# Kernel tuning notes

Hardware: AMD Instinct MI355X
Metric: run time of the kernel (lower is better)

## Reference

```python
import jax, jax.numpy as jnp
from jax import lax
import numpy as np

SEARCH = 9          # search window (asserted == 9 in source)
PAD = SEARCH // 2   # 4
NUM_BINS = 10       # num_dist_bins
BIN_DISP = 0.5      # bin_displacement
NUM_ITER = 3        # num_iter
MIN_FILTER_REG = 1e-5


def _distance_map():
    # DistanceMap: soft-bin the radial distance from the window center.
    c = float(SEARCH // 2)
    yy, xx = jnp.meshgrid(jnp.arange(SEARCH, dtype=jnp.float32),
                          jnp.arange(SEARCH, dtype=jnp.float32), indexing='ij')
    d = jnp.sqrt((yy - c) ** 2 + (xx - c) ** 2) / BIN_DISP          # (9,9)
    k = jnp.arange(NUM_BINS, dtype=jnp.float32)
    bd = d[..., None] - k                                            # (9,9,B)
    vals = jnp.maximum(1.0 - jnp.abs(bd), 0.0)
    last = jnp.clip(bd[..., -1] + 1.0, 0.0, 1.0)                     # saturating last bin
    return vals.at[..., -1].set(last)                                # (9,9,B)


def _local_corr(f, ref_pad, disp):
    # f: (b,c,H,W); ref_pad: (b,c,H+8,W+8) -> scores (b,81,H,W)
    b, c, H, W = f.shape
    def step(_, d):
        r = lax.dynamic_slice(ref_pad, (0, 0, d[0], d[1]), (b, c, H, W))
        return None, jnp.einsum('bchw,bchw->bhw', f, r)
    _, out = lax.scan(step, None, disp)                              # (81,b,H,W)
    return jnp.moveaxis(out, 0, 1)


def _local_corr_t(res, ref_pad, disp):
    # res: (b,81,H,W) -> (b,c,H,W); adjoint of _local_corr w.r.t. the filter arg
    b, c = ref_pad.shape[0], ref_pad.shape[1]
    H, W = res.shape[2], res.shape[3]
    def step(acc, xs):
        d, rd = xs                                                   # rd: (b,H,W)
        r = lax.dynamic_slice(ref_pad, (0, 0, d[0], d[1]), (b, c, H, W))
        return acc + rd[:, None] * r, None
    acc0 = jnp.zeros((b, c, H, W), ref_pad.dtype)
    acc, _ = lax.scan(step, acc0, (disp, jnp.moveaxis(res, 1, 0)))
    return acc


def setup_inputs() -> dict:
    key = jax.random.key(0)
    k1, k2 = jax.random.split(key)
    b, c, H, W = 4, 128, 128, 128
    d = jnp.arange(NUM_BINS, dtype=jnp.float32) * BIN_DISP
    return {
        'filter_map': jax.random.normal(k1, (b, c, H, W), jnp.float32),
        'reference_feat': jax.random.normal(k2, (b, c, H, W), jnp.float32),
        # 1x1-conv predictor weights (num_bins -> 1), at their documented inits:
        'label_w': jnp.exp(-0.5 * d ** 2),            # init_gauss, sigma=1.0
        'spatial_w': jnp.ones((NUM_BINS,), jnp.float32),
        'mask_w': 4.0 * jnp.tanh(2.0 - d),            # v_minus_init_factor * tanh(2 - d)
        'log_step_length': jnp.zeros((1,), jnp.float32),   # log(1.0)
        'filter_reg': 0.01 * jnp.ones((1,), jnp.float32),
    }


def reference(filter_map, reference_feat, label_w, spatial_w, mask_w,
              log_step_length, filter_reg):
    b, c, H, W = filter_map.shape
    dm = _distance_map()                                             # (9,9,B)
    target_map = (dm @ label_w).reshape(1, SEARCH * SEARCH, 1, 1)
    v_plus = (dm @ spatial_w).reshape(1, SEARCH * SEARCH, 1, 1)
    weight_m = jax.nn.sigmoid(dm @ mask_w).reshape(1, SEARCH * SEARCH, 1, 1)

    step_length = jnp.exp(log_step_length).reshape(1, 1, 1, 1)
    reg_weight = jnp.maximum(filter_reg * filter_reg,
                             MIN_FILTER_REG ** 2).reshape(1, 1, 1, 1) / (c * c)

    dys, dxs = jnp.meshgrid(jnp.arange(SEARCH), jnp.arange(SEARCH), indexing='ij')
    disp = jnp.stack([dys.ravel(), dxs.ravel()], axis=1)             # (81,2)
    ref_pad = jnp.pad(reference_feat, ((0, 0), (0, 0), (PAD, PAD), (PAD, PAD)))

    # LeakyReluPar: f(s,a) = (1-a)/2*|s| + (1+a)/2*s ; deriv: (1-a)/2*sign(s) + (1+a)/2
    a_lo = (1.0 - weight_m) * 0.5
    a_hi = (1.0 + weight_m) * 0.5

    f = filter_map
    for _ in range(NUM_ITER):
        scores = _local_corr(f, ref_pad, disp)                       # (b,81,H,W)
        act = v_plus * (a_lo * jnp.abs(scores) + a_hi * scores)
        grad_act = v_plus * (a_lo * jnp.sign(scores) + a_hi)
        residuals = act - v_plus * target_map
        mapped = grad_act * residuals
        f_grad = reg_weight * f + _local_corr_t(mapped, ref_pad, disp)
        sg = grad_act * _local_corr(f_grad, ref_pad, disp)
        alpha_den = jnp.sum(sg * sg, axis=1, keepdims=True)          # (b,1,H,W)
        alpha_num = jnp.sum(f_grad * f_grad, axis=1, keepdims=True)
        alpha = alpha_num / jnp.maximum(alpha_den + reg_weight * alpha_num, 1e-8)
        f = f - step_length * alpha * f_grad
    return f
```

## Files before the change

### kernel.cpp

```cpp
#include <hip/hip_runtime.h>

#define BB 4
#define CC 128
#define HH 128
#define WW 128
#define HW (HH*WW)
#define CHW (CC*HW)
#define ND 81
#define CP 136
#define UPITCH 40
#define PP 32

typedef short s8v __attribute__((ext_vector_type(8)));
typedef short s4v __attribute__((ext_vector_type(4)));
typedef float f4v __attribute__((ext_vector_type(4)));

__device__ __forceinline__ short f2bf(float x){
  unsigned u = __float_as_uint(x);
  unsigned r = (u + 0x7FFFu + ((u >> 16) & 1u)) >> 16;
  return (short)r;
}
__device__ __forceinline__ float bf2f(short s){
  return __uint_as_float(((unsigned)(unsigned short)s) << 16);
}

__global__ void coef_kernel(const float* lw, const float* sw, const float* mw,
                            const float* lsl, const float* fr, float* coef){
  int d = threadIdx.x;
  if (d < ND){
    float dy = (float)(d / 9) - 4.0f;
    float dx = (float)(d % 9) - 4.0f;
    float dist = sqrtf(dy*dy + dx*dx) * 2.0f;
    float t = 0.f, v = 0.f, m = 0.f;
    for (int k = 0; k < 10; k++){
      float bd = dist - (float)k;
      float val = (k == 9) ? fminf(fmaxf(bd + 1.0f, 0.f), 1.f)
                           : fmaxf(1.0f - fabsf(bd), 0.f);
      t += val * lw[k]; v += val * sw[k]; m += val * mw[k];
    }
    float wm = 1.f / (1.f + expf(-m));
    float ah = (1.f + wm) * 0.5f;
    float gp = v, gn = v * wm, gz = v * ah;
    float vt = v * t;
    coef[d]       = gp * gp;
    coef[96+d]    = gn * gn;
    coef[192+d]   = gz * gz;
    coef[288+d]   = gp * vt;
    coef[384+d]   = gn * vt;
    coef[480+d]   = gz * vt;
  }
  if (threadIdx.x == 0){
    coef[576] = expf(lsl[0]);
    float f = fr[0];
    coef[577] = fmaxf(f*f, 1e-10f) / (float)(CC*CC);
  }
}

__global__ __launch_bounds__(256)
void cvt_kernel(const float* ref, short* refT, short* refU){
  __shared__ short T[128*130];
  int r = blockIdx.x, bb = blockIdx.y;
  int tid = threadIdx.x;
  const float* src = ref + (size_t)bb*CHW + (size_t)r*WW;
  short* uout = refU + (size_t)(bb*HH + r) * CC * WW;
  short* tout = refT + (size_t)(bb*HH + r) * WW * CC;
  #pragma unroll
  for (int k = 0; k < 16; k++){
    int q = tid + (k << 8);
    int c = q >> 5, u0 = (q & 31) * 4;
    float4 v = *(const float4*)(src + (size_t)c*HW + u0);
    short h0 = f2bf(v.x), h1 = f2bf(v.y), h2 = f2bf(v.z), h3 = f2bf(v.w);
    s4v pk = {h0, h1, h2, h3};
    *(s4v*)&uout[(size_t)c*WW + u0] = pk;
    T[c*130 + u0 + 0] = h0; T[c*130 + u0 + 1] = h1;
    T[c*130 + u0 + 2] = h2; T[c*130 + u0 + 3] = h3;
  }
  __syncthreads();
  #pragma unroll
  for (int k = 0; k < 16; k++){
    int o = tid + (k << 8);
    int u = o >> 5, c0 = (o & 31) * 4;
    s4v pk = {T[(c0+0)*130 + u], T[(c0+1)*130 + u],
              T[(c0+2)*130 + u], T[(c0+3)*130 + u]};
    *(s4v*)&tout[(size_t)u*CC + c0] = pk;
  }
}

#define L_UC   0
#define L_FGS  8704
#define L_CU   8704
#define L_PM   18944
#define L_CF   26112
#define L_DEN  28672
#define L_NUM  28928
#define L_SA   29184
#define L_SZ   29440

template<int PRE>
__global__ __launch_bounds__(256, 4)
void kF(const float* f_in, const float* ref, const short* refT, const short* refU,
        const float* coef, float* f_out){
  __shared__ char smem[L_SZ];
  short* uc  = (short*)(smem + L_UC);
  short* cu  = (short*)(smem + L_CU);
  short* Pm  = (short*)(smem + L_PM);
  short* fgs = (short*)(smem + L_FGS);
  float* s_cf = (float*)(smem + L_CF);
  float* s_g2 = s_cf;
  float* s_gt = s_cf + 288;
  float* den = (float*)(smem + L_DEN);
  float* num = (float*)(smem + L_NUM);
  float* sa  = (float*)(smem + L_SA);

  int tid = threadIdx.x;
  int lane = tid & 63, wv = tid >> 6;
  int quad = lane >> 4, col = lane & 15;

  int hwid = blockIdx.x + (blockIdx.y << 3) + (blockIdx.z << 8);
  int virt = ((hwid & 7) << 7) + (hwid >> 3);
  int bb = virt >> 8, y0 = ((virt >> 3) & 31) * 4, x0 = (virt & 7) * 16;

  int ub = x0 - 8;

  const float* fimg = f_in + (size_t)bb * CHW;
  const float* rimg = ref  + (size_t)bb * CHW;

  s8v pT0, pT1, pU0, pU1;
  float4 pF0, pF1, pF2, pF3;

  auto loadT = [&](int r){
    if constexpr (PRE){
      const short* tb = refT + (size_t)(bb*HH + r) * WW * CC;
      { int e = tid;       int ua = ub + (e >> 4);
        pT0 = (ua >= 0 && ua < WW)
              ? *(const s8v*)(tb + (size_t)ua*CC + ((e & 15) << 3)) : (s8v)(short)0; }
      { int e = tid + 256; int ua = ub + (e >> 4);
        pT1 = (ua >= 0 && ua < WW)
              ? *(const s8v*)(tb + (size_t)ua*CC + ((e & 15) << 3)) : (s8v)(short)0; }
    } else {
      const float* rb = rimg + (size_t)r * WW;
      float4 z; z.x = z.y = z.z = z.w = 0.f;
      { int e = tid;       int ua = ub + (e & 7)*4;
        pF0 = (ua >= 0 && ua + 4 <= WW) ? *(const float4*)(rb + (size_t)(e >> 3)*HW + ua) : z; }
      { int e = tid + 256; int ua = ub + (e & 7)*4;
        pF1 = (ua >= 0 && ua + 4 <= WW) ? *(const float4*)(rb + (size_t)(e >> 3)*HW + ua) : z; }
      { int e = tid + 512; int ua = ub + (e & 7)*4;
        pF2 = (ua >= 0 && ua + 4 <= WW) ? *(const float4*)(rb + (size_t)(e >> 3)*HW + ua) : z; }
      { int e = tid + 768; int ua = ub + (e & 7)*4;
        pF3 = (ua >= 0 && ua + 4 <= WW) ? *(const float4*)(rb + (size_t)(e >> 3)*HW + ua) : z; }
    }
  };
  auto loadU = [&](int r){
    if constexpr (PRE){
      const short* ubp = refU + (size_t)(bb*HH + r) * CC * WW;
      { int e = tid;       int ua = ub + ((e & 3) << 3);
        pU0 = (ua >= 0 && ua + 8 <= WW)
              ? *(const s8v*)(ubp + (size_t)(e >> 2)*WW + ua) : (s8v)(short)0; }
      { int e = tid + 256; int ua = ub + ((e & 3) << 3);
        pU1 = (ua >= 0 && ua + 8 <= WW)
              ? *(const s8v*)(ubp + (size_t)(e >> 2)*WW + ua) : (s8v)(short)0; }
    }
  };
  auto writeRowA = [&](){
    if constexpr (PRE){
      { int e = tid;       *(s8v*)&uc[(e >> 4)*CP + ((e & 15) << 3)] = pT0; }
      { int e = tid + 256; *(s8v*)&uc[(e >> 4)*CP + ((e & 15) << 3)] = pT1; }
      { int e = tid;       *(s8v*)&cu[(e >> 2)*UPITCH + ((e & 3) << 3)] = pU0; }
      { int e = tid + 256; *(s8v*)&cu[(e >> 2)*UPITCH + ((e & 3) << 3)] = pU1; }
    } else {
      float4 vv[4] = {pF0, pF1, pF2, pF3};
      #pragma unroll
      for (int k = 0; k < 4; k++){
        int e4 = tid + (k << 8);
        int u4 = (e4 & 7) * 4, c = e4 >> 3;
        short h0 = f2bf(vv[k].x), h1 = f2bf(vv[k].y),
              h2 = f2bf(vv[k].z), h3 = f2bf(vv[k].w);
        uc[(u4+0)*CP + c] = h0; uc[(u4+1)*CP + c] = h1;
        uc[(u4+2)*CP + c] = h2; uc[(u4+3)*CP + c] = h3;
        s4v pk = {h0, h1, h2, h3};
        *(s4v*)&cu[c*UPITCH + u4] = pk;
      }
    }
  };
  auto writeRowB = [&](){
    if constexpr (PRE){
      { int e = tid;       *(s8v*)&uc[(e >> 4)*CP + ((e & 15) << 3)] = pT0; }
      { int e = tid + 256; *(s8v*)&uc[(e >> 4)*CP + ((e & 15) << 3)] = pT1; }
    } else {
      float4 vv[4] = {pF0, pF1, pF2, pF3};
      #pragma unroll
      for (int k = 0; k < 4; k++){
        int e4 = tid + (k << 8);
        int u4 = (e4 & 7) * 4, c = e4 >> 3;
        uc[(u4+0)*CP + c] = f2bf(vv[k].x); uc[(u4+1)*CP + c] = f2bf(vv[k].y);
        uc[(u4+2)*CP + c] = f2bf(vv[k].z); uc[(u4+3)*CP + c] = f2bf(vv[k].w);
      }
    }
  };

  if (y0 - 4 >= 0){ loadT(y0 - 4); loadU(y0 - 4); }

  for (int e = tid; e < 640; e += 256) s_cf[e] = coef[e];

  int fy = y0 + wv;
  s8v a_hi[4], a_lo[4];
  #pragma unroll
  for (int kc = 0; kc < 4; kc++){
    short th[8], tl[8];
    #pragma unroll
    for (int j = 0; j < 8; j++){
      int c = kc*32 + quad*8 + j;
      float v = fimg[(size_t)c * HW + fy * WW + x0 + col];
      short h = f2bf(v);
      th[j] = h; tl[j] = f2bf(v - bf2f(h));
    }
    a_hi[kc] = *(const s8v*)th;
    a_lo[kc] = *(const s8v*)tl;
  }

  f4v D[8];
  #pragma unroll
  for (int i = 0; i < 8; i++) D[i] = (f4v)0.f;

  unsigned long long f0 = 0ull, f1 = 0ull, f2 = 0ull;

  for (int rr = 0; rr < 12; rr++){
    int r = y0 + rr - 4;
    bool rv = (r >= 0) && (r < HH);
    __syncthreads();
    if (rv) writeRowA();
    __syncthreads();
    if (rr < 11){
      int rn = r + 1;
      if (rn >= 0 && rn < HH){ loadT(rn); loadU(rn); }
    }
    int dy = rr - wv;
    if (dy >= 0 && dy <= 8){
      unsigned pack = 0u;
      if (rv){
        f4v C0 = (f4v)0.f, C1 = (f4v)0.f;
        #pragma unroll
        for (int kc = 0; kc < 4; kc++){
          s8v b0 = *(const s8v*)&uc[col*CP      + kc*32 + quad*8];
          s8v b1 = *(const s8v*)&uc[(16+col)*CP + kc*32 + quad*8];
          C0 = __builtin_amdgcn_mfma_f32_16x16x32_bf16(a_hi[kc], b0, C0, 0,0,0);
          C0 = __builtin_amdgcn_mfma_f32_16x16x32_bf16(a_lo[kc], b0, C0, 0,0,0);
          C1 = __builtin_amdgcn_mfma_f32_16x16x32_bf16(a_hi[kc], b1, C1, 0,0,0);
          C1 = __builtin_amdgcn_mfma_f32_16x16x32_bf16(a_lo[kc], b1, C1, 0,0,0);
        }
        #pragma unroll
        for (int nt = 0; nt < 2; nt++){
          f4v Cv = nt ? C1 : C0;
          #pragma unroll
          for (int reg = 0; reg < 4; reg++){
            int x  = quad*4 + reg;
            int up = nt*16 + col;
            int dxm = up - x - 4;
            float m = 0.f;
            if ((unsigned)dxm <= 8u){
              float s = Cv[reg];
              int d = dy*9 + dxm;
              unsigned pos = (s > 0.f) ? 1u : 0u;
              unsigned neg = (s < 0.f) ? 1u : 0u;
              int off = pos ? 0 : (neg ? 96 : 192);
              float g2 = s_g2[off + d];
              float gt = s_gt[off + d];
              m = fmaf(g2, s, -gt);
              pack |= (pos | (neg << 1)) << ((nt*4 + reg) * 2);
            }
            Pm[(wv*16 + x)*PP + up] = f2bf(m);
          }
        }
        asm volatile("s_waitcnt lgkmcnt(0)" ::: "memory");
        __builtin_amdgcn_sched_barrier(0);
        s8v pa = *(const s8v*)&Pm[(wv*16 + col)*PP + quad*8];
        #pragma unroll
        for (int ct = 0; ct < 8; ct++){
          s8v bc = *(const s8v*)&cu[(ct*16 + col)*UPITCH + quad*8];
          D[ct] = __builtin_amdgcn_mfma_f32_16x16x32_bf16(pa, bc, D[ct], 0,0,0);
        }
      }
      f0 = (f0 >> 16) | (f1 << 48);
      f1 = (f1 >> 16) | (f2 << 48);
      f2 = (f2 >> 16) | ((unsigned long long)pack << 48);
    }
  }

  if (y0 - 4 >= 0) loadT(y0 - 4);

  float rw = s_cf[577];
  __syncthreads();
  #pragma unroll
  for (int ct = 0; ct < 8; ct++){
    #pragma unroll
    for (int reg = 0; reg < 4; reg++){
      int x = quad*4 + reg, c = ct*16 + col;
      float fv = fimg[(size_t)c * HW + fy * WW + x0 + x];
      fgs[(wv*16 + x)*CP + c] = f2bf(D[ct][reg] + rw * fv);
    }
  }
  __syncthreads();
  if (tid < 64){
    float s = 0.f;
    #pragma unroll
    for (int kc = 0; kc < 16; kc++){
      s8v v = *(const s8v*)&fgs[tid*CP + kc*8];
      #pragma unroll
      for (int j = 0; j < 8; j++){ float f = bf2f(v[j]); s += f*f; }
    }
    num[tid] = s;
  }

  s8v ga_[4];
  #pragma unroll
  for (int kc = 0; kc < 4; kc++)
    ga_[kc] = *(const s8v*)&fgs[(wv*16 + col)*CP + kc*32 + quad*8];

  float dacc[4] = {0.f, 0.f, 0.f, 0.f};

  for (int rr = 0; rr < 12; rr++){
    int r = y0 + rr - 4;
    bool rv = (r >= 0) && (r < HH);
    __syncthreads();
    if (rv) writeRowB();
    __syncthreads();
    if (rr < 11){
      int rn = r + 1;
      if (rn >= 0 && rn < HH) loadT(rn);
    }
    int dy = rr - wv;
    if (dy >= 0 && dy <= 8){
      unsigned pack = (unsigned)(f0 >> 48) & 0xFFFFu;
      f0 = (f0 >> 16) | (f1 << 48);
      f1 = (f1 >> 16) | (f2 << 48);
      f2 >>= 16;
      if (rv){
        f4v C0 = (f4v)0.f, C1 = (f4v)0.f;
        #pragma unroll
        for (int kc = 0; kc < 4; kc++){
          s8v b0 = *(const s8v*)&uc[col*CP      + kc*32 + quad*8];
          s8v b1 = *(const s8v*)&uc[(16+col)*CP + kc*32 + quad*8];
          C0 = __builtin_amdgcn_mfma_f32_16x16x32_bf16(ga_[kc], b0, C0, 0,0,0);
          C1 = __builtin_amdgcn_mfma_f32_16x16x32_bf16(ga_[kc], b1, C1, 0,0,0);
        }
        #pragma unroll
        for (int nt = 0; nt < 2; nt++){
          f4v Cv = nt ? C1 : C0;
          #pragma unroll
          for (int reg = 0; reg < 4; reg++){
            int x  = quad*4 + reg;
            int up = nt*16 + col;
            int dxm = up - x - 4;
            if ((unsigned)dxm <= 8u){
              int d = dy*9 + dxm;
              unsigned b2 = pack >> ((nt*4 + reg) * 2);
              int off = (b2 & 1u) ? 0 : ((b2 & 2u) ? 96 : 192);
              float g2 = s_g2[off + d];
              float t  = Cv[reg];
              dacc[reg] = fmaf(g2 * t, t, dacc[reg]);
            }
          }
        }
      }
    }
  }

  #pragma unroll
  for (int reg = 0; reg < 4; reg++){
    float v = dacc[reg];
    v += __shfl_xor(v, 1);
    v += __shfl_xor(v, 2);
    v += __shfl_xor(v, 4);
    v += __shfl_xor(v, 8);
    if (col == 0) den[wv*16 + quad*4 + reg] = v;
  }

  __syncthreads();
  if (tid < 64){
    float step = s_cf[576];
    float alpha = num[tid] / fmaxf(den[tid] + rw*num[tid], 1e-8f);
    sa[tid] = step * alpha;
  }
  __syncthreads();

  float* oimg = f_out + (size_t)bb * CHW;
  for (int e = tid; e < 8192; e += 256){
    int x = e & 15, y = (e >> 4) & 3, c = e >> 6;
    size_t gi = (size_t)c * HW + (y0 + y) * WW + x0 + x;
    float v = fimg[gi] - sa[y*16 + x] * bf2f(fgs[(y*16 + x)*CP + c]);
    oimg[gi] = v;
  }
}

extern "C" void kernel_launch(void* const* d_in, const int* in_sizes, int n_in,
                              void* d_out, int out_size, void* d_ws, size_t ws_size,
                              hipStream_t stream) {
  const float* filter_map = (const float*)d_in[0];
  const float* ref        = (const float*)d_in[1];
  const float* label_w    = (const float*)d_in[2];
  const float* spatial_w  = (const float*)d_in[3];
  const float* mask_w     = (const float*)d_in[4];
  const float* lsl        = (const float*)d_in[5];
  const float* freg       = (const float*)d_in[6];

  float* coef = (float*)d_ws;
  float* fbuf = (float*)d_out;

  short* refT = (short*)((char*)d_ws + 65536);
  short* refU = refT + (size_t)BB * CHW;
  size_t need = 65536 + 2 * (size_t)BB * CHW * sizeof(short);
  bool pre = (ws_size >= need);

  coef_kernel<<<dim3(1), dim3(128), 0, stream>>>(label_w, spatial_w, mask_w, lsl, freg, coef);
  if (pre)
    cvt_kernel<<<dim3(HH, BB), dim3(256), 0, stream>>>(ref, refT, refU);

  dim3 grid(8, 32, BB);
  for (int it = 0; it < 3; it++){
    const float* fsrc = (it == 0) ? filter_map : (const float*)fbuf;
    if (pre) kF<1><<<grid, 256, 0, stream>>>(fsrc, ref, refT, refU, coef, fbuf);
    else     kF<0><<<grid, 256, 0, stream>>>(fsrc, ref, refT, refU, coef, fbuf);
  }
}
```

Before: 335.5 us.

## Enlarge spatial tile to 8 rows with 512-thread blocks and interleave coefficients

Each block now covers 8 output rows instead of 4, using 8 waves and 512 threads, so every staged reference row is reused by twice as many output rows. The halo overhead drops from 12 staged rows per 4 outputs to 16 per 8. Coefficients are repacked so g2 and gt for each displacement and sign case sit together and load as one float2. The block count halves and LDS per block grows (e.g. PP padding), which lowers block-level parallelism and occupancy per CU.

```diff
diff --git a/kernel.cpp b/kernel.cpp
--- a/kernel.cpp
+++ b/kernel.cpp
@@ -9,7 +9,7 @@
 #define ND 81
 #define CP 136
 #define UPITCH 40
-#define PP 32
+#define PP 40
 
 typedef short s8v __attribute__((ext_vector_type(8)));
 typedef short s4v __attribute__((ext_vector_type(4)));
@@ -42,17 +42,14 @@
     float ah = (1.f + wm) * 0.5f;
     float gp = v, gn = v * wm, gz = v * ah;
     float vt = v * t;
-    coef[d]       = gp * gp;
-    coef[96+d]    = gn * gn;
-    coef[192+d]   = gz * gz;
-    coef[288+d]   = gp * vt;
-    coef[384+d]   = gn * vt;
-    coef[480+d]   = gz * vt;
+    coef[(d*3+0)*2+0] = gp * gp;  coef[(d*3+0)*2+1] = gp * vt;
+    coef[(d*3+1)*2+0] = gn * gn;  coef[(d*3+1)*2+1] = gn * vt;
+    coef[(d*3+2)*2+0] = gz * gz;  coef[(d*3+2)*2+1] = gz * vt;
   }
   if (threadIdx.x == 0){
-    coef[576] = expf(lsl[0]);
+    coef[500] = expf(lsl[0]);
     float f = fr[0];
-    coef[577] = fmaxf(f*f, 1e-10f) / (float)(CC*CC);
+    coef[501] = fmaxf(f*f, 1e-10f) / (float)(CC*CC);
   }
 }
 
@@ -90,14 +87,14 @@
 #define L_FGS  8704
 #define L_CU   8704
 #define L_PM   18944
-#define L_CF   26112
-#define L_DEN  28672
-#define L_NUM  28928
-#define L_SA   29184
-#define L_SZ   29440
+#define L_CF   43520
+#define L_DEN  45568
+#define L_NUM  46080
+#define L_SA   46592
+#define L_SZ   47104
 
 template<int PRE>
-__global__ __launch_bounds__(256, 4)
+__global__ __launch_bounds__(512, 6)
 void kF(const float* f_in, const float* ref, const short* refT, const short* refU,
         const float* coef, float* f_out){
   __shared__ char smem[L_SZ];
@@ -106,8 +103,6 @@
   short* Pm  = (short*)(smem + L_PM);
   short* fgs = (short*)(smem + L_FGS);
   float* s_cf = (float*)(smem + L_CF);
-  float* s_g2 = s_cf;
-  float* s_gt = s_cf + 288;
   float* den = (float*)(smem + L_DEN);
   float* num = (float*)(smem + L_NUM);
   float* sa  = (float*)(smem + L_SA);
@@ -116,62 +111,50 @@
   int lane = tid & 63, wv = tid >> 6;
   int quad = lane >> 4, col = lane & 15;
 
-  int hwid = blockIdx.x + (blockIdx.y << 3) + (blockIdx.z << 8);
-  int virt = ((hwid & 7) << 7) + (hwid >> 3);
-  int bb = virt >> 8, y0 = ((virt >> 3) & 31) * 4, x0 = (virt & 7) * 16;
+  int hwid = blockIdx.x + (blockIdx.y << 3) + (blockIdx.z << 7);
+  int virt = ((hwid & 7) << 6) + (hwid >> 3);
+  int bb = virt >> 7, y0 = ((virt >> 3) & 15) * 8, x0 = (virt & 7) * 16;
 
   int ub = x0 - 8;
 
   const float* fimg = f_in + (size_t)bb * CHW;
   const float* rimg = ref  + (size_t)bb * CHW;
 
-  s8v pT0, pT1, pU0, pU1;
-  float4 pF0, pF1, pF2, pF3;
+  s8v pT0, pU0;
+  float4 pF0, pF1;
 
   auto loadT = [&](int r){
     if constexpr (PRE){
       const short* tb = refT + (size_t)(bb*HH + r) * WW * CC;
-      { int e = tid;       int ua = ub + (e >> 4);
-        pT0 = (ua >= 0 && ua < WW)
-              ? *(const s8v*)(tb + (size_t)ua*CC + ((e & 15) << 3)) : (s8v)(short)0; }
-      { int e = tid + 256; int ua = ub + (e >> 4);
-        pT1 = (ua >= 0 && ua < WW)
-              ? *(const s8v*)(tb + (size_t)ua*CC + ((e & 15) << 3)) : (s8v)(short)0; }
+      int ua = ub + (tid >> 4);
+      pT0 = (ua >= 0 && ua < WW)
+            ? *(const s8v*)(tb + (size_t)ua*CC + ((tid & 15) << 3)) : (s8v)(short)0;
     } else {
       const float* rb = rimg + (size_t)r * WW;
       float4 z; z.x = z.y = z.z = z.w = 0.f;
       { int e = tid;       int ua = ub + (e & 7)*4;
         pF0 = (ua >= 0 && ua + 4 <= WW) ? *(const float4*)(rb + (size_t)(e >> 3)*HW + ua) : z; }
-      { int e = tid + 256; int ua = ub + (e & 7)*4;
+      { int e = tid + 512; int ua = ub + (e & 7)*4;
         pF1 = (ua >= 0 && ua + 4 <= WW) ? *(const float4*)(rb + (size_t)(e >> 3)*HW + ua) : z; }
-      { int e = tid + 512; int ua = ub + (e & 7)*4;
-        pF2 = (ua >= 0 && ua + 4 <= WW) ? *(const float4*)(rb + (size_t)(e >> 3)*HW + ua) : z; }
-      { int e = tid + 768; int ua = ub + (e & 7)*4;
-        pF3 = (ua >= 0 && ua + 4 <= WW) ? *(const float4*)(rb + (size_t)(e >> 3)*HW + ua) : z; }
     }
   };
   auto loadU = [&](int r){
     if constexpr (PRE){
       const short* ubp = refU + (size_t)(bb*HH + r) * CC * WW;
-      { int e = tid;       int ua = ub + ((e & 3) << 3);
-        pU0 = (ua >= 0 && ua + 8 <= WW)
-              ? *(const s8v*)(ubp + (size_t)(e >> 2)*WW + ua) : (s8v)(short)0; }
-      { int e = tid + 256; int ua = ub + ((e & 3) << 3);
-        pU1 = (ua >= 0 && ua + 8 <= WW)
-              ? *(const s8v*)(ubp + (size_t)(e >> 2)*WW + ua) : (s8v)(short)0; }
+      int ua = ub + ((tid & 3) << 3);
+      pU0 = (ua >= 0 && ua + 8 <= WW)
+            ? *(const s8v*)(ubp + (size_t)(tid >> 2)*WW + ua) : (s8v)(short)0;
     }
   };
   auto writeRowA = [&](){
     if constexpr (PRE){
-      { int e = tid;       *(s8v*)&uc[(e >> 4)*CP + ((e & 15) << 3)] = pT0; }
-      { int e = tid + 256; *(s8v*)&uc[(e >> 4)*CP + ((e & 15) << 3)] = pT1; }
-      { int e = tid;       *(s8v*)&cu[(e >> 2)*UPITCH + ((e & 3) << 3)] = pU0; }
-      { int e = tid + 256; *(s8v*)&cu[(e >> 2)*UPITCH + ((e & 3) << 3)] = pU1; }
+      *(s8v*)&uc[(tid >> 4)*CP + ((tid & 15) << 3)] = pT0;
+      *(s8v*)&cu[(tid >> 2)*UPITCH + ((tid & 3) << 3)] = pU0;
     } else {
-      float4 vv[4] = {pF0, pF1, pF2, pF3};
+      float4 vv[2] = {pF0, pF1};
       #pragma unroll
-      for (int k = 0; k < 4; k++){
-        int e4 = tid + (k << 8);
+      for (int k = 0; k < 2; k++){
+        int e4 = tid + (k << 9);
         int u4 = (e4 & 7) * 4, c = e4 >> 3;
         short h0 = f2bf(vv[k].x), h1 = f2bf(vv[k].y),
               h2 = f2bf(vv[k].z), h3 = f2bf(vv[k].w);
@@ -184,13 +167,12 @@
   };
   auto writeRowB = [&](){
     if constexpr (PRE){
-      { int e = tid;       *(s8v*)&uc[(e >> 4)*CP + ((e & 15) << 3)] = pT0; }
-      { int e = tid + 256; *(s8v*)&uc[(e >> 4)*CP + ((e & 15) << 3)] = pT1; }
+      *(s8v*)&uc[(tid >> 4)*CP + ((tid & 15) << 3)] = pT0;
     } else {
-      float4 vv[4] = {pF0, pF1, pF2, pF3};
+      float4 vv[2] = {pF0, pF1};
       #pragma unroll
-      for (int k = 0; k < 4; k++){
-        int e4 = tid + (k << 8);
+      for (int k = 0; k < 2; k++){
+        int e4 = tid + (k << 9);
         int u4 = (e4 & 7) * 4, c = e4 >> 3;
         uc[(u4+0)*CP + c] = f2bf(vv[k].x); uc[(u4+1)*CP + c] = f2bf(vv[k].y);
         uc[(u4+2)*CP + c] = f2bf(vv[k].z); uc[(u4+3)*CP + c] = f2bf(vv[k].w);
@@ -200,7 +182,7 @@
 
   if (y0 - 4 >= 0){ loadT(y0 - 4); loadU(y0 - 4); }
 
-  for (int e = tid; e < 640; e += 256) s_cf[e] = coef[e];
+  if (tid < 512) s_cf[tid] = coef[tid];
 
   int fy = y0 + wv;
   s8v a_hi[4], a_lo[4];
@@ -224,13 +206,13 @@
 
   unsigned long long f0 = 0ull, f1 = 0ull, f2 = 0ull;
 
-  for (int rr = 0; rr < 12; rr++){
+  for (int rr = 0; rr < 16; rr++){
     int r = y0 + rr - 4;
     bool rv = (r >= 0) && (r < HH);
     __syncthreads();
     if (rv) writeRowA();
     __syncthreads();
-    if (rr < 11){
+    if (rr < 15){
       int rn = r + 1;
       if (rn >= 0 && rn < HH){ loadT(rn); loadU(rn); }
     }
@@ -262,10 +244,9 @@
               int d = dy*9 + dxm;
               unsigned pos = (s > 0.f) ? 1u : 0u;
               unsigned neg = (s < 0.f) ? 1u : 0u;
-              int off = pos ? 0 : (neg ? 96 : 192);
-              float g2 = s_g2[off + d];
-              float gt = s_gt[off + d];
-              m = fmaf(g2, s, -gt);
+              int cse = pos ? 0 : (neg ? 1 : 2);
+              float2 gg = *(const float2*)&s_cf[(d*3 + cse)*2];
+              m = fmaf(gg.x, s, -gg.y);
               pack |= (pos | (neg << 1)) << ((nt*4 + reg) * 2);
             }
             Pm[(wv*16 + x)*PP + up] = f2bf(m);
@@ -288,7 +269,7 @@
 
   if (y0 - 4 >= 0) loadT(y0 - 4);
 
-  float rw = s_cf[577];
+  float rw = s_cf[501];
   __syncthreads();
   #pragma unroll
   for (int ct = 0; ct < 8; ct++){
@@ -300,15 +281,18 @@
     }
   }
   __syncthreads();
-  if (tid < 64){
+  {
+    int px = tid >> 2, k4 = (tid & 3) * 4;
     float s = 0.f;
     #pragma unroll
-    for (int kc = 0; kc < 16; kc++){
-      s8v v = *(const s8v*)&fgs[tid*CP + kc*8];
+    for (int j = 0; j < 4; j++){
+      s8v v = *(const s8v*)&fgs[px*CP + (k4 + j)*8];
       #pragma unroll
-      for (int j = 0; j < 8; j++){ float f = bf2f(v[j]); s += f*f; }
-    }
-    num[tid] = s;
+      for (int jj = 0; jj < 8; jj++){ float f = bf2f(v[jj]); s += f*f; }
+    }
+    s += __shfl_xor(s, 1);
+    s += __shfl_xor(s, 2);
+    if ((tid & 3) == 0) num[px] = s;
   }
 
   s8v ga_[4];
@@ -318,13 +302,13 @@
 
   float dacc[4] = {0.f, 0.f, 0.f, 0.f};
 
-  for (int rr = 0; rr < 12; rr++){
+  for (int rr = 0; rr < 16; rr++){
     int r = y0 + rr - 4;
     bool rv = (r >= 0) && (r < HH);
     __syncthreads();
     if (rv) writeRowB();
     __syncthreads();
-    if (rr < 11){
+    if (rr < 15){
       int rn = r + 1;
       if (rn >= 0 && rn < HH) loadT(rn);
     }
@@ -354,8 +338,8 @@
             if ((unsigned)dxm <= 8u){
               int d = dy*9 + dxm;
               unsigned b2 = pack >> ((nt*4 + reg) * 2);
-              int off = (b2 & 1u) ? 0 : ((b2 & 2u) ? 96 : 192);
-              float g2 = s_g2[off + d];
+              int cse = (b2 & 1u) ? 0 : ((b2 & 2u) ? 1 : 2);
+              float g2 = s_cf[(d*3 + cse)*2];
               float t  = Cv[reg];
               dacc[reg] = fmaf(g2 * t, t, dacc[reg]);
             }
@@ -376,16 +360,16 @@
   }
 
   __syncthreads();
-  if (tid < 64){
-    float step = s_cf[576];
+  if (tid < 128){
+    float step = s_cf[500];
     float alpha = num[tid] / fmaxf(den[tid] + rw*num[tid], 1e-8f);
     sa[tid] = step * alpha;
   }
   __syncthreads();
 
   float* oimg = f_out + (size_t)bb * CHW;
-  for (int e = tid; e < 8192; e += 256){
-    int x = e & 15, y = (e >> 4) & 3, c = e >> 6;
+  for (int e = tid; e < 16384; e += 512){
+    int x = e & 15, y = (e >> 4) & 7, c = e >> 7;
     size_t gi = (size_t)c * HW + (y0 + y) * WW + x0 + x;
     float v = fimg[gi] - sa[y*16 + x] * bf2f(fgs[(y*16 + x)*CP + c]);
     oimg[gi] = v;
@@ -415,10 +399,10 @@
   if (pre)
     cvt_kernel<<<dim3(HH, BB), dim3(256), 0, stream>>>(ref, refT, refU);
 
-  dim3 grid(8, 32, BB);
+  dim3 grid(8, 16, BB);
   for (int it = 0; it < 3; it++){
     const float* fsrc = (it == 0) ? filter_map : (const float*)fbuf;
-    if (pre) kF<1><<<grid, 256, 0, stream>>>(fsrc, ref, refT, refU, coef, fbuf);
-    else     kF<0><<<grid, 256, 0, stream>>>(fsrc, ref, refT, refU, coef, fbuf);
-  }
-}
+    if (pre) kF<1><<<grid, 512, 0, stream>>>(fsrc, ref, refT, refU, coef, fbuf);
+    else     kF<0><<<grid, 512, 0, stream>>>(fsrc, ref, refT, refU, coef, fbuf);
+  }
+}
```

After: 587.1 us. 1.75x slower.
